# Kernel tuning notes

Measured on AMD Instinct MI355X. Metric: run time of the kernel, lower is better.

## Reference

```python
import jax, jax.numpy as jnp
import numpy as np

H = 8; D = 128; HD = D // H; T = 6; N = 512; E = 16384; FIN = 15; L = 3


def _ln(v, g, b, eps=1e-5):
    m = v.mean(-1, keepdims=True)
    var = ((v - m) ** 2).mean(-1, keepdims=True)
    return (v - m) / jnp.sqrt(var + eps) * g + b


def _gat(xn, src, dst, W, a_src, a_dst, b):
    # PyG GATConv, concat=False: lin (no bias) -> per-edge LeakyReLU scores ->
    # segment softmax over incoming edges -> scatter-sum -> head mean -> bias.
    h = (xn @ W).reshape(N, H, D)  # [N, H, D]
    e = jax.nn.leaky_relu((h * a_src).sum(-1)[src] + (h * a_dst).sum(-1)[dst], 0.2)  # [E+N, H]
    m = jax.ops.segment_max(e, dst, num_segments=N)
    ex = jnp.exp(e - m[dst])
    s = jax.ops.segment_sum(ex, dst, num_segments=N)
    a = ex / s[dst]
    out = jax.ops.segment_sum(a[..., None] * h[src], dst, num_segments=N)  # [N, H, D]
    return out.mean(1) + b


def _forward(x, edge_index, gat_W, gat_asrc, gat_adst, gat_b, ln_g, ln_b,
             enc_Wqkv, enc_bqkv, enc_Wo, enc_bo, enc_ln1g, enc_ln1b,
             enc_W1, enc_b1, enc_W2, enc_b2, enc_ln2g, enc_ln2b,
             risk_W1, risk_b1, risk_W2, risk_b2,
             mode_W1, mode_b1, mode_W2, mode_b2,
             unc_W1, unc_b1, unc_W2, unc_b2):
    B = x.shape[0]  # 1
    ar = jnp.arange(N)
    src = jnp.concatenate([edge_index[0], ar])  # PyG add_self_loops=True
    dst = jnp.concatenate([edge_index[1], ar])
    gat_t = jax.vmap(lambda xt: _gat(xt, src, dst, gat_W, gat_asrc, gat_adst, gat_b))(x[0])  # [T,N,D]
    sp = _ln(gat_t, ln_g, ln_b)
    h = sp.reshape(B, T * N, D)
    S = T * N
    for l in range(L):  # nn.TransformerEncoder, post-norm, ReLU FFN, eval mode
        qkv = h @ enc_Wqkv[l] + enc_bqkv[l]
        q, k, v = jnp.split(qkv, 3, axis=-1)
        q = q.reshape(B, S, H, HD); k = k.reshape(B, S, H, HD); v = v.reshape(B, S, H, HD)
        att = jax.nn.softmax(jnp.einsum('bqhd,bkhd->bhqk', q, k) / np.sqrt(HD).astype(np.float32), axis=-1)
        o = jnp.einsum('bhqk,bkhd->bqhd', att, v).reshape(B, S, D) @ enc_Wo[l] + enc_bo[l]
        h = _ln(h + o, enc_ln1g[l], enc_ln1b[l])
        f = jax.nn.relu(h @ enc_W1[l] + enc_b1[l]) @ enc_W2[l] + enc_b2[l]
        h = _ln(h + f, enc_ln2g[l], enc_ln2b[l])
    g = h.mean(1)  # [B, D]
    risk = jax.nn.sigmoid(jax.nn.relu(g @ risk_W1 + risk_b1) @ risk_W2 + risk_b2).squeeze()
    mode = jax.nn.relu(g @ mode_W1 + mode_b1) @ mode_W2 + mode_b2
    unc = jax.nn.softplus(jax.nn.relu(g @ unc_W1 + unc_b1) @ unc_W2 + unc_b2)
    return risk, mode, unc


def setup_inputs() -> dict:
    key = jax.random.key(0)
    ks = jax.random.split(key, 20)
    def w(i, shape, s=0.05):
        return (s * jax.random.normal(ks[i], shape)).astype(jnp.float32)
    return dict(
        x=jax.random.normal(ks[0], (1, T, N, FIN), jnp.float32),
        edge_index=jax.random.randint(ks[1], (2, E), 0, N, dtype=jnp.int32),
        gat_W=w(2, (FIN, H * D)),
        gat_asrc=w(3, (H, D)), gat_adst=w(4, (H, D)), gat_b=jnp.zeros((D,), jnp.float32),
        ln_g=jnp.ones((D,), jnp.float32), ln_b=jnp.zeros((D,), jnp.float32),
        enc_Wqkv=w(5, (L, D, 3 * D)), enc_bqkv=jnp.zeros((L, 3 * D), jnp.float32),
        enc_Wo=w(6, (L, D, D)), enc_bo=jnp.zeros((L, D), jnp.float32),
        enc_ln1g=jnp.ones((L, D), jnp.float32), enc_ln1b=jnp.zeros((L, D), jnp.float32),
        enc_W1=w(7, (L, D, 2048)), enc_b1=jnp.zeros((L, 2048), jnp.float32),
        enc_W2=w(8, (L, 2048, D)), enc_b2=jnp.zeros((L, D), jnp.float32),
        enc_ln2g=jnp.ones((L, D), jnp.float32), enc_ln2b=jnp.zeros((L, D), jnp.float32),
        risk_W1=w(9, (D, 64)), risk_b1=jnp.zeros((64,), jnp.float32),
        risk_W2=w(10, (64, 1)), risk_b2=jnp.zeros((1,), jnp.float32),
        mode_W1=w(11, (D, 32)), mode_b1=jnp.zeros((32,), jnp.float32),
        mode_W2=w(12, (32, 8)), mode_b2=jnp.zeros((8,), jnp.float32),
        unc_W1=w(13, (D, 32)), unc_b1=jnp.zeros((32,), jnp.float32),
        unc_W2=w(14, (32, 2)), unc_b2=jnp.zeros((2,), jnp.float32),
    )


def reference(x, edge_index, gat_W, gat_asrc, gat_adst, gat_b, ln_g, ln_b,
              enc_Wqkv, enc_bqkv, enc_Wo, enc_bo, enc_ln1g, enc_ln1b,
              enc_W1, enc_b1, enc_W2, enc_b2, enc_ln2g, enc_ln2b,
              risk_W1, risk_b1, risk_W2, risk_b2,
              mode_W1, mode_b1, mode_W2, mode_b2,
              unc_W1, unc_b1, unc_W2, unc_b2):
    return _forward(x, edge_index, gat_W, gat_asrc, gat_adst, gat_b, ln_g, ln_b,
                    enc_Wqkv, enc_bqkv, enc_Wo, enc_bo, enc_ln1g, enc_ln1b,
                    enc_W1, enc_b1, enc_W2, enc_b2, enc_ln2g, enc_ln2b,
                    risk_W1, risk_b1, risk_W2, risk_b2,
                    mode_W1, mode_b1, mode_W2, mode_b2,
                    unc_W1, unc_b1, unc_W2, unc_b2)
```

## Files before the change

kernel.cpp:

```cpp
#include <hip/hip_runtime.h>
#include <hip/hip_bf16.h>
#include <math.h>

#define T 6
#define N 512
#define E 16384
#define EN (E + N)
#define H 8
#define D 128
#define HD 16
#define S (T * N)
#define FIN 15
#define FF 2048
#define KS 4
#define FCH 8
#define GCH 64
#define SM_SHIFT2 2.88539008f
#define QSCALE 0.36067376f
#define VPAD2 136

typedef _Float16 half_t;
typedef _Float16 half8 __attribute__((ext_vector_type(8)));
typedef _Float16 half4 __attribute__((ext_vector_type(4)));
typedef float f32x4 __attribute__((ext_vector_type(4)));

#define MFMA16(a, b, c) __builtin_amdgcn_mfma_f32_16x16x32_f16(a, b, c, 0, 0, 0)
#define MFMA16K16(a, b, c) __builtin_amdgcn_mfma_f32_16x16x16f16(a, b, c, 0, 0, 0)

#define O_A      0
#define O_EBUF   (T*N*H*D)
#define O_C      (O_EBUF + T*EN*H)
#define O_HSEQ   (O_C + T*N*H*D)
#define O_OBUF   (O_HSEQ + S*D)
#define O_SSRC   (O_OBUF + S*D)
#define O_SDST   (O_SSRC + T*N*H)
#define O_SEGM   (O_SDST + T*N*H)
#define O_SEGS   (O_SEGM + T*N*H)
#define O_INT    (O_SEGS + T*N*H)
#define O_G      (O_INT + 20000)

#define I_DEG    0
#define I_START  512
#define I_CURS   1025
#define I_CSRE   1537

#define WB_OFF   (3*H*S*HD)
#define WB_QKV   0
#define WB_WO    147456
#define WB_W1    196608
#define WB_W2    983040

__device__ __forceinline__ float bsum(float v, float* lds, int nw) {
    #pragma unroll
    for (int off = 32; off > 0; off >>= 1) v += __shfl_down(v, off, 64);
    int w = threadIdx.x >> 6;
    if ((threadIdx.x & 63) == 0) lds[w] = v;
    __syncthreads();
    float r = 0.f;
    for (int i = 0; i < nw; ++i) r += lds[i];
    __syncthreads();
    return r;
}

__device__ __forceinline__ half_t* swz_ptr(half_t* base, int token, int col) {
    int byte = token * 256 + col * 2;
    byte ^= (token & 7) << 4;
    return (half_t*)((char*)base + byte);
}
__device__ __forceinline__ half_t* swz_ptr256(half_t* base, int token, int col) {
    int byte = token * 512 + col * 2;
    byte ^= (token & 7) << 4;
    return (half_t*)((char*)base + byte);
}

__global__ void init_kernel(float* g, int* ia) {
    int i = blockIdx.x * blockDim.x + threadIdx.x;
    if (i < D) g[i] = 0.f;
    if (i < N) ia[I_DEG + i] = 0;
}

__global__ __launch_bounds__(256) void gat_lin_kernel(
        const float* __restrict__ x, const float* __restrict__ W,
        const float* __restrict__ asrc, const float* __restrict__ adst,
        half_t* __restrict__ hbuf16, float* __restrict__ ssrc, float* __restrict__ sdst) {
    int r = blockIdx.x;
    int tid = threadIdx.x;
    __shared__ float xr[FIN];
    __shared__ float hl[H*D];
    if (tid < FIN) xr[tid] = x[r * FIN + tid];
    __syncthreads();
    #pragma unroll
    for (int kk = 0; kk < 4; ++kk) {
        int col = tid + kk * 256;
        float acc = 0.f;
        #pragma unroll
        for (int f = 0; f < FIN; ++f) acc += xr[f] * W[f * (H*D) + col];
        hbuf16[(size_t)r * (H*D) + col] = (half_t)acc;
        hl[col] = acc;
    }
    __syncthreads();
    int w = tid >> 6, lane = tid & 63;
    #pragma unroll
    for (int i = 0; i < 4; ++i) {
        int p = w*4 + i;
        int head = p >> 1;
        const float* av = ((p & 1) ? adst : asrc) + head * D;
        float v = hl[head*D + lane] * av[lane] + hl[head*D + 64 + lane] * av[64 + lane];
        #pragma unroll
        for (int off = 32; off > 0; off >>= 1) v += __shfl_down(v, off, 64);
        if (lane == 0) {
            if (p & 1) sdst[r*H + head] = v;
            else       ssrc[r*H + head] = v;
        }
    }
}

__global__ void csr_count_kernel(const int* __restrict__ ei, int* ia) {
    int j = blockIdx.x * blockDim.x + threadIdx.x;
    if (j >= EN) return;
    int dn = (j < E) ? ei[E + j] : (j - E);
    atomicAdd(&ia[I_DEG + dn], 1);
}

__global__ void csr_scan_kernel(int* ia) {
    __shared__ int buf[N];
    int tid = threadIdx.x;
    int v = ia[I_DEG + tid];
    buf[tid] = v;
    __syncthreads();
    for (int off = 1; off < N; off <<= 1) {
        int t = (tid >= off) ? buf[tid - off] : 0;
        __syncthreads();
        buf[tid] += t;
        __syncthreads();
    }
    ia[I_START + tid + 1] = buf[tid];
    if (tid == 0) ia[I_START] = 0;
    ia[I_CURS + tid] = buf[tid] - v;
}

__global__ void csr_fill_kernel(const int* __restrict__ ei, int* ia) {
    int j = blockIdx.x * blockDim.x + threadIdx.x;
    if (j >= EN) return;
    int dn = (j < E) ? ei[E + j] : (j - E);
    int slot = atomicAdd(&ia[I_CURS + dn], 1);
    ia[I_CSRE + slot] = j;
}

__global__ __launch_bounds__(128) void gat_fused_kernel(
        const int* __restrict__ ei, const int* __restrict__ ia,
        const float* __restrict__ ssrc, const float* __restrict__ sdst,
        const half_t* __restrict__ hbuf16, const float* __restrict__ gb,
        const float* __restrict__ lng, const float* __restrict__ lnb,
        float* __restrict__ hseq) {
    int bid = blockIdx.x;
    int wg = (bid & 7) * (T*N/8) + (bid >> 3);
    int t = wg / N, n = wg % N;
    int tid = threadIdx.x;
    int myh = tid & 7;

    __shared__ int snarr[GCH];
    __shared__ float earr[GCH][H];
    __shared__ float red[128];
    __shared__ float sdl[H], mS[H], sS[H], scl[H];
    __shared__ float lnred[2];

    if (tid < H) {
        sdl[tid] = sdst[(t*N + n)*H + tid];
        mS[tid] = -3.0e38f;
        sS[tid] = 0.f;
    }
    float acc[H];
    #pragma unroll
    for (int h = 0; h < H; ++h) acc[h] = 0.f;
    int e0 = ia[I_START + n], e1 = ia[I_START + n + 1];
    __syncthreads();

    for (int c0 = e0; c0 < e1; c0 += GCH) {
        int cn = min(GCH, e1 - c0);
        if (tid < cn) {
            int j = ia[I_CSRE + c0 + tid];
            snarr[tid] = (j < E) ? ei[j] : (j - E);
        }
        __syncthreads();
        float lm = -3.0e38f;
        for (int w = tid; w < cn*H; w += 128) {
            int ce = w >> 3;
            float e = ssrc[(t*N + snarr[ce])*H + myh] + sdl[myh];
            e = (e > 0.f) ? e : 0.2f * e;
            earr[ce][myh] = e;
            lm = fmaxf(lm, e);
        }
        red[tid] = lm;
        __syncthreads();
        if (tid < H) {
            float cm = red[tid];
            #pragma unroll
            for (int k = 1; k < 16; ++k) cm = fmaxf(cm, red[tid + 8*k]);
            float mn = fmaxf(mS[tid], cm);
            scl[tid] = __expf(mS[tid] - mn);
            mS[tid] = mn;
        }
        __syncthreads();
        float ls = 0.f;
        float mh = mS[myh];
        for (int w = tid; w < cn*H; w += 128) {
            int ce = w >> 3;
            float p = __expf(earr[ce][myh] - mh);
            earr[ce][myh] = p;
            ls += p;
        }
        red[tid] = ls;
        __syncthreads();
        if (tid < H) {
            float cs = red[tid];
            #pragma unroll
            for (int k = 1; k < 16; ++k) cs += red[tid + 8*k];
            sS[tid] = sS[tid] * scl[tid] + cs;
        }
        #pragma unroll
        for (int h = 0; h < H; ++h) acc[h] *= scl[h];
        for (int ce = 0; ce < cn; ++ce) {
            const half_t* hp = hbuf16 + ((size_t)(t*N + snarr[ce]) * H) * D + tid;
            #pragma unroll
            for (int h = 0; h < H; ++h)
                acc[h] += earr[ce][h] * (float)hp[(size_t)h * D];
        }
        __syncthreads();
    }

    float v = 0.f;
    #pragma unroll
    for (int h = 0; h < H; ++h) v += acc[h] / sS[h];
    v = v * (1.f / H) + gb[tid];
    float mean = bsum(v, lnred, 2) * (1.f / D);
    float diff = v - mean;
    float var = bsum(diff * diff, lnred, 2) * (1.f / D);
    hseq[(size_t)(t*N + n) * D + tid] = diff * rsqrtf(var + 1e-5f) * lng[tid] + lnb[tid];
}

__global__ __launch_bounds__(256) void wconv_kernel(
        const float* __restrict__ Wqkv, const float* __restrict__ Wo,
        const float* __restrict__ W1, const float* __restrict__ W2,
        half_t* __restrict__ WqkvT, half_t* __restrict__ WoT,
        half_t* __restrict__ W1T, half_t* __restrict__ W2T) {
    int b = blockIdx.x;
    int l = b / 576, r = b % 576;
    const float* src; half_t* dst; int Rr, Cc, tr, tc;
    if (r < 48)       { src = Wqkv + (size_t)l*128*384;  dst = WqkvT + (size_t)l*384*128;  Rr=128;  Cc=384;  tc = r % 12;        tr = r / 12; }
    else if (r < 64)  { int rr=r-48;  src = Wo + (size_t)l*128*128;  dst = WoT + (size_t)l*128*128;  Rr=128;  Cc=128;  tc = rr % 4;  tr = rr / 4; }
    else if (r < 320) { int rr=r-64;  src = W1 + (size_t)l*128*2048; dst = W1T + (size_t)l*2048*128; Rr=128;  Cc=2048; tc = rr % 64; tr = rr / 64; }
    else              { int rr=r-320; src = W2 + (size_t)l*2048*128; dst = W2T + (size_t)l*128*2048; Rr=2048; Cc=128;  tc = rr % 4;  tr = rr / 4; }
    __shared__ float t[32][33];
    int tx = threadIdx.x & 31, ty = threadIdx.x >> 5;
    #pragma unroll
    for (int i = 0; i < 4; ++i) {
        int row = tr*32 + ty + i*8, col = tc*32 + tx;
        t[ty + i*8][tx] = src[(size_t)row * Cc + col];
    }
    __syncthreads();
    #pragma unroll
    for (int i = 0; i < 4; ++i) {
        int orow = tc*32 + ty + i*8, ocol = tr*32 + tx;
        dst[(size_t)orow * Rr + ocol] = (half_t)t[tx][ty + i*8];
    }
}

__global__ __launch_bounds__(256) void qkv_mfma_kernel(
        const float* __restrict__ hseq, const half_t* __restrict__ WqkvT,
        const float* __restrict__ bqkv,
        half_t* __restrict__ Qh, half_t* __restrict__ Kh, half_t* __restrict__ Vt) {
    __shared__ half_t xt[32*128];
    int tid = threadIdx.x;
    int s0 = blockIdx.x * 32;
    for (int c = tid; c < 512; c += 256) {
        int token = c >> 4, col8 = (c & 15) * 8;
        const float* src = hseq + (size_t)(s0 + token) * 128 + col8;
        float4 a = *(const float4*)src;
        float4 b = *(const float4*)(src + 4);
        half8 v;
        v[0]=(half_t)a.x; v[1]=(half_t)a.y; v[2]=(half_t)a.z; v[3]=(half_t)a.w;
        v[4]=(half_t)b.x; v[5]=(half_t)b.y; v[6]=(half_t)b.z; v[7]=(half_t)b.w;
        *(half8*)swz_ptr(xt, token, col8) = v;
    }
    __syncthreads();
    int lane = tid & 63, w = tid >> 6;
    int lr = lane & 15, lg = lane >> 4;
    f32x4 acc[6][2];
    #pragma unroll
    for (int m = 0; m < 6; ++m)
        #pragma unroll
        for (int n = 0; n < 2; ++n) acc[m][n] = (f32x4){0.f, 0.f, 0.f, 0.f};
    #pragma unroll
    for (int ks = 0; ks < 4; ++ks) {
        half8 bf[2];
        #pragma unroll
        for (int n = 0; n < 2; ++n)
            bf[n] = *(half8*)swz_ptr(xt, n*16 + lr, ks*32 + lg*8);
        #pragma unroll
        for (int m = 0; m < 6; ++m) {
            int row = w*96 + m*16 + lr;
            half8 af = *(const half8*)(WqkvT + (size_t)row*128 + ks*32 + lg*8);
            #pragma unroll
            for (int n = 0; n < 2; ++n) acc[m][n] = MFMA16(af, bf[n], acc[m][n]);
        }
    }
    #pragma unroll
    for (int m = 0; m < 6; ++m) {
        int qd = w*96 + m*16 + lg*4;
        float4 bb = *(const float4*)(bqkv + qd);
        int part = qd >> 7, c = qd & 127, head = c >> 4, dd = c & 15;
        #pragma unroll
        for (int n = 0; n < 2; ++n) {
            int token = n*16 + lr;
            float v0 = acc[m][n][0] + bb.x, v1 = acc[m][n][1] + bb.y;
            float v2 = acc[m][n][2] + bb.z, v3 = acc[m][n][3] + bb.w;
            if (part == 0) {
                half4 hv = { (half_t)(v0*QSCALE), (half_t)(v1*QSCALE),
                             (half_t)(v2*QSCALE), (half_t)(v3*QSCALE) };
                *(half4*)(Qh + ((size_t)head*S + s0 + token)*HD + dd) = hv;
            } else if (part == 1) {
                half4 hv = { (half_t)v0, (half_t)v1, (half_t)v2, (half_t)v3 };
                *(half4*)(Kh + ((size_t)head*S + s0 + token)*HD + dd) = hv;
            } else {
                Vt[((size_t)head*HD + dd + 0)*S + s0 + token] = (half_t)v0;
                Vt[((size_t)head*HD + dd + 1)*S + s0 + token] = (half_t)v1;
                Vt[((size_t)head*HD + dd + 2)*S + s0 + token] = (half_t)v2;
                Vt[((size_t)head*HD + dd + 3)*S + s0 + token] = (half_t)v3;
            }
        }
    }
}

__global__ __launch_bounds__(256) void attn7_kernel(
        const half_t* __restrict__ Qh, const half_t* __restrict__ Kh,
        const half_t* __restrict__ Vt, float* __restrict__ pacc,
        float* __restrict__ pl) {
    int qb = blockIdx.x, h = blockIdx.y, ks = blockIdx.z;
    int tid = threadIdx.x;
    int lane = tid & 63;
    int w = tid >> 6;
    int lr = lane & 15, lg = lane >> 4;
    int qg0 = qb*128 + w*32 + lr;
    int qg1 = qg0 + 16;
    const f32x4 zf = {0.f, 0.f, 0.f, 0.f};

    __shared__ half_t kbuf[2][128*16];
    __shared__ half_t vbuf[2][16*VPAD2];

    half4 qf0 = *(const half4*)(Qh + ((size_t)h*S + qg0)*HD + lg*4);
    half4 qf1 = *(const half4*)(Qh + ((size_t)h*S + qg1)*HD + lg*4);

    int krow = tid >> 1, kch = tid & 1;
    int vdim = tid >> 4, vch = tid & 15;
    const half_t* Kbase = Kh + (size_t)h*S*HD;
    const half_t* Vbase = Vt + (size_t)h*HD*S;
    int kb0 = ks*(S/KS);

    *(half8*)&kbuf[0][krow*16 + kch*8] = *(const half8*)(Kbase + (size_t)(kb0+krow)*HD + kch*8);
    *(half8*)&vbuf[0][vdim*VPAD2 + vch*8] = *(const half8*)(Vbase + (size_t)vdim*S + kb0 + vch*8);
    __syncthreads();

    float l0 = 0.f, l1 = 0.f;
    f32x4 oa0 = zf, oa1 = zf, ob0 = zf, ob1 = zf;
    int cur = 0;
    const int NT = (S/KS)/128;
    for (int t = 0; t < NT; ++t) {
        int tn = (t+1 < NT) ? (t+1) : t;
        int kbn = kb0 + tn*128;
        half8 knext = *(const half8*)(Kbase + (size_t)(kbn+krow)*HD + kch*8);
        half8 vnext = *(const half8*)(Vbase + (size_t)vdim*S + kbn + vch*8);

        f32x4 sc0[8], sc1[8];
        #pragma unroll
        for (int ct = 0; ct < 8; ++ct) {
            half4 kf = *(half4*)&kbuf[cur][(ct*16+lr)*16 + lg*4];
            sc0[ct] = MFMA16K16(kf, qf0, zf);
            sc1[ct] = MFMA16K16(kf, qf1, zf);
        }
        half4 pf0[8], pf1[8];
        #pragma unroll
        for (int ct = 0; ct < 8; ++ct)
            #pragma unroll
            for (int r = 0; r < 4; ++r) {
                float pv0 = exp2f(sc0[ct][r] - SM_SHIFT2);
                float pv1 = exp2f(sc1[ct][r] - SM_SHIFT2);
                l0 += pv0; l1 += pv1;
                pf0[ct][r] = (half_t)pv0;
                pf1[ct][r] = (half_t)pv1;
            }
        #pragma unroll
        for (int ct = 0; ct < 8; ++ct) {
            half4 vf = *(half4*)&vbuf[cur][lr*VPAD2 + ct*16 + lg*4];
            if (ct & 1) { oa1 = MFMA16K16(vf, pf0[ct], oa1); ob1 = MFMA16K16(vf, pf1[ct], ob1); }
            else        { oa0 = MFMA16K16(vf, pf0[ct], oa0); ob0 = MFMA16K16(vf, pf1[ct], ob0); }
        }
        *(half8*)&kbuf[cur^1][krow*16 + kch*8] = knext;
        *(half8*)&vbuf[cur^1][vdim*VPAD2 + vch*8] = vnext;
        __syncthreads();
        cur ^= 1;
    }
    oa0[0]+=oa1[0]; oa0[1]+=oa1[1]; oa0[2]+=oa1[2]; oa0[3]+=oa1[3];
    ob0[0]+=ob1[0]; ob0[1]+=ob1[1]; ob0[2]+=ob1[2]; ob0[3]+=ob1[3];

    l0 += __shfl_xor(l0, 16, 64); l0 += __shfl_xor(l0, 32, 64);
    l1 += __shfl_xor(l1, 16, 64); l1 += __shfl_xor(l1, 32, 64);

    size_t oi0 = ((size_t)(ks*H + h) * S + qg0);
    size_t oi1 = ((size_t)(ks*H + h) * S + qg1);
    if (lg == 0) { pl[oi0] = l0; pl[oi1] = l1; }
    #pragma unroll
    for (int r = 0; r < 4; ++r) {
        pacc[oi0 * HD + lg*4 + r] = oa0[r];
        pacc[oi1 * HD + lg*4 + r] = ob0[r];
    }
}

__global__ __launch_bounds__(256) void oproj_mfma_ln_kernel(
        const float* __restrict__ pacc, const float* __restrict__ pl,
        const half_t* __restrict__ WoT,
        const float* __restrict__ bo, const float* __restrict__ lng,
        const float* __restrict__ lnb, float* __restrict__ hseq) {
    __shared__ half_t xt[32*128];
    __shared__ float yt[32*132];
    int tid = threadIdx.x;
    int s0 = blockIdx.x * 32;
    for (int c = tid; c < 512; c += 256) {
        int token = c >> 4, col8 = (c & 15) * 8;
        int s = s0 + token;
        int h = col8 >> 4, dd0 = col8 & 15;
        float L = 0.f;
        float a[8] = {0,0,0,0,0,0,0,0};
        #pragma unroll
        for (int k = 0; k < KS; ++k) {
            size_t oi = ((size_t)(k*H + h) * S + s);
            L += pl[oi];
            const float* pp = pacc + oi * HD + dd0;
            float4 p0 = *(const float4*)pp;
            float4 p1 = *(const float4*)(pp + 4);
            a[0]+=p0.x; a[1]+=p0.y; a[2]+=p0.z; a[3]+=p0.w;
            a[4]+=p1.x; a[5]+=p1.y; a[6]+=p1.z; a[7]+=p1.w;
        }
        float inv = 1.f / L;
        half8 v;
        #pragma unroll
        for (int i = 0; i < 8; ++i) v[i] = (half_t)(a[i] * inv);
        *(half8*)swz_ptr(xt, token, col8) = v;
    }
    __syncthreads();
    int lane = tid & 63, w = tid >> 6;
    int lr = lane & 15, lg = lane >> 4;
    f32x4 acc[2][2];
    #pragma unroll
    for (int m = 0; m < 2; ++m)
        #pragma unroll
        for (int n = 0; n < 2; ++n) acc[m][n] = (f32x4){0.f, 0.f, 0.f, 0.f};
    #pragma unroll
    for (int kk = 0; kk < 4; ++kk) {
        half8 bf[2];
        #pragma unroll
        for (int n = 0; n < 2; ++n)
            bf[n] = *(half8*)swz_ptr(xt, n*16 + lr, kk*32 + lg*8);
        #pragma unroll
        for (int m = 0; m < 2; ++m) {
            int row = w*32 + m*16 + lr;
            half8 af = *(const half8*)(WoT + (size_t)row*128 + kk*32 + lg*8);
            #pragma unroll
            for (int n = 0; n < 2; ++n) acc[m][n] = MFMA16(af, bf[n], acc[m][n]);
        }
    }
    #pragma unroll
    for (int m = 0; m < 2; ++m)
        #pragma unroll
        for (int n = 0; n < 2; ++n) {
            int token = n*16 + lr;
            int od = w*32 + m*16 + lg*4;
            *(f32x4*)&yt[token*132 + od] = acc[m][n];
        }
    __syncthreads();
    {
        int token = tid >> 3, part = tid & 7;
        const float* hres = hseq + (size_t)(s0 + token) * 128;
        float v[16];
        float sum = 0.f;
        #pragma unroll
        for (int i = 0; i < 16; ++i) {
            int dim = part*16 + i;
            v[i] = yt[token*132 + dim] + bo[dim] + hres[dim];
            sum += v[i];
        }
        sum += __shfl_xor(sum, 1, 64); sum += __shfl_xor(sum, 2, 64); sum += __shfl_xor(sum, 4, 64);
        float mean = sum * (1.f/128.f);
        float vs = 0.f;
        #pragma unroll
        for (int i = 0; i < 16; ++i) { float dq = v[i] - mean; vs += dq*dq; }
        vs += __shfl_xor(vs, 1, 64); vs += __shfl_xor(vs, 2, 64); vs += __shfl_xor(vs, 4, 64);
        float inv = rsqrtf(vs * (1.f/128.f) + 1e-5f);
        #pragma unroll
        for (int i = 0; i < 16; ++i) {
            int dim = part*16 + i;
            hseq[(size_t)(s0+token)*128 + dim] = (v[i]-mean)*inv*lng[dim] + lnb[dim];
        }
    }
}

__global__ __launch_bounds__(256) void ffn_mfma2_kernel(
        const half_t* __restrict__ W1T, const half_t* __restrict__ W2T,
        const float* __restrict__ b1, const float* __restrict__ hseq,
        float* __restrict__ ypart) {
    __shared__ half_t xt[32*128];
    __shared__ half_t h1[32*256];
    int tid = threadIdx.x;
    int s0 = blockIdx.x * 32;
    int fc = blockIdx.y;
    int fbase = fc * 256;
    for (int c = tid; c < 512; c += 256) {
        int token = c >> 4, col8 = (c & 15) * 8;
        const float* src = hseq + (size_t)(s0 + token) * 128 + col8;
        float4 a = *(const float4*)src;
        float4 b = *(const float4*)(src + 4);
        half8 v;
        v[0]=(half_t)a.x; v[1]=(half_t)a.y; v[2]=(half_t)a.z; v[3]=(half_t)a.w;
        v[4]=(half_t)b.x; v[5]=(half_t)b.y; v[6]=(half_t)b.z; v[7]=(half_t)b.w;
        *(half8*)swz_ptr(xt, token, col8) = v;
    }
    __syncthreads();
    int lane = tid & 63, mw = tid >> 6;
    int lr = lane & 15, lg = lane >> 4;

    f32x4 hacc[4][2];
    #pragma unroll
    for (int m = 0; m < 4; ++m)
        #pragma unroll
        for (int n = 0; n < 2; ++n) hacc[m][n] = (f32x4){0.f, 0.f, 0.f, 0.f};
    #pragma unroll
    for (int ksx = 0; ksx < 4; ++ksx) {
        half8 bf[2];
        #pragma unroll
        for (int n = 0; n < 2; ++n)
            bf[n] = *(half8*)swz_ptr(xt, n*16 + lr, ksx*32 + lg*8);
        #pragma unroll
        for (int m = 0; m < 4; ++m) {
            int row = fbase + mw*64 + m*16 + lr;
            half8 af = *(const half8*)(W1T + (size_t)row*128 + ksx*32 + lg*8);
            #pragma unroll
            for (int n = 0; n < 2; ++n) hacc[m][n] = MFMA16(af, bf[n], hacc[m][n]);
        }
    }
    #pragma unroll
    for (int m = 0; m < 4; ++m) {
        int frow = mw*64 + m*16 + lg*4;
        float4 bb = *(const float4*)(b1 + fbase + frow);
        #pragma unroll
        for (int n = 0; n < 2; ++n) {
            int token = n*16 + lr;
            half4 hv;
            hv[0] = (half_t)fmaxf(hacc[m][n][0] + bb.x, 0.f);
            hv[1] = (half_t)fmaxf(hacc[m][n][1] + bb.y, 0.f);
            hv[2] = (half_t)fmaxf(hacc[m][n][2] + bb.z, 0.f);
            hv[3] = (half_t)fmaxf(hacc[m][n][3] + bb.w, 0.f);
            *(half4*)swz_ptr256(h1, token, frow) = hv;
        }
    }
    __syncthreads();

    f32x4 yacc[2][2];
    #pragma unroll
    for (int m = 0; m < 2; ++m)
        #pragma unroll
        for (int n = 0; n < 2; ++n) yacc[m][n] = (f32x4){0.f, 0.f, 0.f, 0.f};
    #pragma unroll
    for (int ksx = 0; ksx < 8; ++ksx) {
        half8 bf[2];
        #pragma unroll
        for (int n = 0; n < 2; ++n)
            bf[n] = *(half8*)swz_ptr256(h1, n*16 + lr, ksx*32 + lg*8);
        #pragma unroll
        for (int m = 0; m < 2; ++m) {
            int row = mw*32 + m*16 + lr;
            half8 af = *(const half8*)(W2T + (size_t)row*2048 + fbase + ksx*32 + lg*8);
            #pragma unroll
            for (int n = 0; n < 2; ++n) yacc[m][n] = MFMA16(af, bf[n], yacc[m][n]);
        }
    }
    #pragma unroll
    for (int m = 0; m < 2; ++m)
        #pragma unroll
        for (int n = 0; n < 2; ++n) {
            int token = n*16 + lr;
            int od = mw*32 + m*16 + lg*4;
            *(f32x4*)&ypart[((size_t)fc*S + s0 + token)*128 + od] = yacc[m][n];
        }
}

__global__ __launch_bounds__(256) void ffn_reduce_ln_kernel(
        const float* __restrict__ ypart, const float* __restrict__ b2,
        const float* __restrict__ lng, const float* __restrict__ lnb,
        float* __restrict__ hseq) {
    int tid = threadIdx.x;
    int token = blockIdx.x * 64 + (tid >> 2);
    int part = tid & 3;
    const float* hres = hseq + (size_t)token * 128;
    float v[32];
    #pragma unroll
    for (int i = 0; i < 32; ++i) {
        int dim = part*32 + i;
        v[i] = b2[dim] + hres[dim];
    }
    #pragma unroll
    for (int fcc = 0; fcc < FCH; ++fcc) {
        const float* yp = ypart + ((size_t)fcc*S + token)*128 + part*32;
        #pragma unroll
        for (int i = 0; i < 32; ++i) v[i] += yp[i];
    }
    float sum = 0.f;
    #pragma unroll
    for (int i = 0; i < 32; ++i) sum += v[i];
    sum += __shfl_xor(sum, 1, 64); sum += __shfl_xor(sum, 2, 64);
    float mean = sum * (1.f/128.f);
    float vs = 0.f;
    #pragma unroll
    for (int i = 0; i < 32; ++i) { float dq = v[i] - mean; vs += dq*dq; }
    vs += __shfl_xor(vs, 1, 64); vs += __shfl_xor(vs, 2, 64);
    float inv = rsqrtf(vs * (1.f/128.f) + 1e-5f);
    #pragma unroll
    for (int i = 0; i < 32; ++i) {
        int dim = part*32 + i;
        hseq[(size_t)token*128 + dim] = (v[i]-mean)*inv*lng[dim] + lnb[dim];
    }
}

__global__ void pool_kernel(const float* __restrict__ hseq, float* __restrict__ g) {
    int d = threadIdx.x;
    int b = blockIdx.x;
    float acc = 0.f;
    for (int s = b * 128; s < (b + 1) * 128; ++s) acc += hseq[s * D + d];
    atomicAdd(&g[d], acc * (1.f / S));
}

__global__ void heads_kernel(const float* __restrict__ g,
                             const float* __restrict__ rW1, const float* __restrict__ rb1,
                             const float* __restrict__ rW2, const float* __restrict__ rb2,
                             const float* __restrict__ mW1, const float* __restrict__ mb1,
                             const float* __restrict__ mW2, const float* __restrict__ mb2,
                             const float* __restrict__ uW1, const float* __restrict__ ub1,
                             const float* __restrict__ uW2, const float* __restrict__ ub2,
                             float* __restrict__ out) {
    int tid = threadIdx.x;
    __shared__ float gl[D];
    __shared__ float r1[64];
    __shared__ float mh[32];
    __shared__ float uh[32];
    gl[tid] = g[tid];
    gl[tid + 64] = g[tid + 64];
    __syncthreads();
    {
        float acc = rb1[tid];
        for (int k = 0; k < D; ++k) acc += gl[k] * rW1[k * 64 + tid];
        r1[tid] = fmaxf(acc, 0.f);
    }
    if (tid < 32) {
        float am = mb1[tid], au = ub1[tid];
        for (int k = 0; k < D; ++k) {
            am += gl[k] * mW1[k * 32 + tid];
            au += gl[k] * uW1[k * 32 + tid];
        }
        mh[tid] = fmaxf(am, 0.f);
        uh[tid] = fmaxf(au, 0.f);
    }
    __syncthreads();
    if (tid == 0) {
        float acc = rb2[0];
        for (int k = 0; k < 64; ++k) acc += r1[k] * rW2[k];
        out[0] = 1.f / (1.f + __expf(-acc));
    }
    if (tid < 8) {
        float acc = mb2[tid];
        for (int k = 0; k < 32; ++k) acc += mh[k] * mW2[k * 8 + tid];
        out[1 + tid] = acc;
    }
    if (tid < 2) {
        float acc = ub2[tid];
        for (int k = 0; k < 32; ++k) acc += uh[k] * uW2[k * 2 + tid];
        out[9 + tid] = (acc > 20.f) ? acc : log1pf(__expf(acc));
    }
}

extern "C" void kernel_launch(void* const* d_in, const int* in_sizes, int n_in,
                              void* d_out, int out_size, void* d_ws, size_t ws_size,
                              hipStream_t stream) {
    const float* x       = (const float*)d_in[0];
    const int*   ei      = (const int*)  d_in[1];
    const float* gat_W   = (const float*)d_in[2];
    const float* gat_asrc= (const float*)d_in[3];
    const float* gat_adst= (const float*)d_in[4];
    const float* gat_b   = (const float*)d_in[5];
    const float* ln_g    = (const float*)d_in[6];
    const float* ln_b    = (const float*)d_in[7];
    const float* Wqkv    = (const float*)d_in[8];
    const float* bqkv    = (const float*)d_in[9];
    const float* Wo      = (const float*)d_in[10];
    const float* bo      = (const float*)d_in[11];
    const float* ln1g    = (const float*)d_in[12];
    const float* ln1b    = (const float*)d_in[13];
    const float* W1      = (const float*)d_in[14];
    const float* b1      = (const float*)d_in[15];
    const float* W2      = (const float*)d_in[16];
    const float* b2      = (const float*)d_in[17];
    const float* ln2g    = (const float*)d_in[18];
    const float* ln2b    = (const float*)d_in[19];
    const float* rW1     = (const float*)d_in[20];
    const float* rb1     = (const float*)d_in[21];
    const float* rW2     = (const float*)d_in[22];
    const float* rb2     = (const float*)d_in[23];
    const float* mW1     = (const float*)d_in[24];
    const float* mb1     = (const float*)d_in[25];
    const float* mW2     = (const float*)d_in[26];
    const float* mb2     = (const float*)d_in[27];
    const float* uW1     = (const float*)d_in[28];
    const float* ub1     = (const float*)d_in[29];
    const float* uW2     = (const float*)d_in[30];
    const float* ub2     = (const float*)d_in[31];

    float* ws = (float*)d_ws;
    half_t*       hbuf16 = (half_t*)(ws + O_A);
    half_t*       Qh   = (half_t*)(ws + O_A);
    half_t*       Kh   = Qh + (size_t)H*S*HD;
    half_t*       Vt   = Kh + (size_t)H*S*HD;
    half_t*       wb   = (half_t*)(ws + O_A + WB_OFF);
    half_t*       WqkvT= wb + WB_QKV;
    half_t*       WoT  = wb + WB_WO;
    half_t*       W1T  = wb + WB_W1;
    half_t*       W2T  = wb + WB_W2;
    float*        pacc = ws + O_C;
    float*        ypart= ws + O_C;
    float*        pl   = ws + O_C + (size_t)KS*H*S*HD;
    float*        hseq = ws + O_HSEQ;
    float*        ssrc = ws + O_SSRC;
    float*        sdst = ws + O_SDST;
    int*          ia   = (int*)(ws + O_INT);
    float*        gvec = ws + O_G;
    float* out = (float*)d_out;

    init_kernel<<<dim3(2), dim3(256), 0, stream>>>(gvec, ia);

    gat_lin_kernel<<<dim3(T*N), dim3(256), 0, stream>>>(x, gat_W, gat_asrc, gat_adst,
                                                        hbuf16, ssrc, sdst);
    csr_count_kernel<<<dim3((EN + 255) / 256), dim3(256), 0, stream>>>(ei, ia);
    csr_scan_kernel<<<dim3(1), dim3(N), 0, stream>>>(ia);
    csr_fill_kernel<<<dim3((EN + 255) / 256), dim3(256), 0, stream>>>(ei, ia);
    gat_fused_kernel<<<dim3(T*N), dim3(128), 0, stream>>>(
        ei, ia, ssrc, sdst, hbuf16, gat_b, ln_g, ln_b, hseq);

    wconv_kernel<<<dim3(3*576), dim3(256), 0, stream>>>(Wqkv, Wo, W1, W2, WqkvT, WoT, W1T, W2T);

    for (int l = 0; l < 3; ++l) {
        qkv_mfma_kernel<<<dim3(S/32), dim3(256), 0, stream>>>(
            hseq, WqkvT + (size_t)l*384*128, bqkv + l*3*D, Qh, Kh, Vt);
        attn7_kernel<<<dim3(S/128, H, KS), dim3(256), 0, stream>>>(Qh, Kh, Vt, pacc, pl);
        oproj_mfma_ln_kernel<<<dim3(S/32), dim3(256), 0, stream>>>(
            pacc, pl, WoT + (size_t)l*128*128, bo + l*D, ln1g + l*D, ln1b + l*D, hseq);
        ffn_mfma2_kernel<<<dim3(S/32, FCH), dim3(256), 0, stream>>>(
            W1T + (size_t)l*2048*128, W2T + (size_t)l*128*2048,
            b1 + l*FF, hseq, ypart);
        ffn_reduce_ln_kernel<<<dim3(S/64), dim3(256), 0, stream>>>(
            ypart, b2 + l*D, ln2g + l*D, ln2b + l*D, hseq);
    }

    pool_kernel<<<dim3(S / 128), dim3(128), 0, stream>>>(hseq, gvec);
    heads_kernel<<<dim3(1), dim3(64), 0, stream>>>(gvec, rW1, rb1, rW2, rb2,
                                                   mW1, mb1, mW2, mb2,
                                                   uW1, ub1, uW2, ub2, out);
}
```

Measured before the change: 332.8 us.

## Fuse FFN reduce+LayerNorm into next QKV kernel and CSR count into GAT linear

Measured after the change: 303.2 us. 1.1x faster.

```diff
diff --git a/kernel.cpp b/kernel.cpp
--- a/kernel.cpp
+++ b/kernel.cpp
@@ -82,9 +82,15 @@
 __global__ __launch_bounds__(256) void gat_lin_kernel(
         const float* __restrict__ x, const float* __restrict__ W,
         const float* __restrict__ asrc, const float* __restrict__ adst,
+        const int* __restrict__ ei, int* __restrict__ ia,
         half_t* __restrict__ hbuf16, float* __restrict__ ssrc, float* __restrict__ sdst) {
     int r = blockIdx.x;
     int tid = threadIdx.x;
+    int j = r * 256 + tid;
+    if (r < (EN + 255) / 256 && j < EN) {
+        int dn = (j < E) ? ei[E + j] : (j - E);
+        atomicAdd(&ia[I_DEG + dn], 1);
+    }
     __shared__ float xr[FIN];
     __shared__ float hl[H*D];
     if (tid < FIN) xr[tid] = x[r * FIN + tid];
@@ -113,13 +119,6 @@
             else       ssrc[r*H + head] = v;
         }
     }
-}
-
-__global__ void csr_count_kernel(const int* __restrict__ ei, int* ia) {
-    int j = blockIdx.x * blockDim.x + threadIdx.x;
-    if (j >= EN) return;
-    int dn = (j < E) ? ei[E + j] : (j - E);
-    atomicAdd(&ia[I_DEG + dn], 1);
 }
 
 __global__ void csr_scan_kernel(int* ia) {
@@ -267,21 +266,58 @@
 }
 
 __global__ __launch_bounds__(256) void qkv_mfma_kernel(
-        const float* __restrict__ hseq, const half_t* __restrict__ WqkvT,
-        const float* __restrict__ bqkv,
+        float* __restrict__ hseq, const float* __restrict__ ypart,
+        const float* __restrict__ b2, const float* __restrict__ lng2,
+        const float* __restrict__ lnb2, int doRed,
+        const half_t* __restrict__ WqkvT, const float* __restrict__ bqkv,
         half_t* __restrict__ Qh, half_t* __restrict__ Kh, half_t* __restrict__ Vt) {
     __shared__ half_t xt[32*128];
     int tid = threadIdx.x;
     int s0 = blockIdx.x * 32;
-    for (int c = tid; c < 512; c += 256) {
-        int token = c >> 4, col8 = (c & 15) * 8;
-        const float* src = hseq + (size_t)(s0 + token) * 128 + col8;
-        float4 a = *(const float4*)src;
-        float4 b = *(const float4*)(src + 4);
-        half8 v;
-        v[0]=(half_t)a.x; v[1]=(half_t)a.y; v[2]=(half_t)a.z; v[3]=(half_t)a.w;
-        v[4]=(half_t)b.x; v[5]=(half_t)b.y; v[6]=(half_t)b.z; v[7]=(half_t)b.w;
-        *(half8*)swz_ptr(xt, token, col8) = v;
+    if (doRed) {
+        int token = tid >> 3, part = tid & 7;
+        int s = s0 + token;
+        const float* hres = hseq + (size_t)s * 128;
+        float v[16];
+        #pragma unroll
+        for (int i = 0; i < 16; ++i) v[i] = b2[part*16 + i] + hres[part*16 + i];
+        #pragma unroll
+        for (int fcc = 0; fcc < FCH; ++fcc) {
+            const float* yp = ypart + ((size_t)fcc*S + s)*128 + part*16;
+            #pragma unroll
+            for (int i = 0; i < 16; ++i) v[i] += yp[i];
+        }
+        float sum = 0.f;
+        #pragma unroll
+        for (int i = 0; i < 16; ++i) sum += v[i];
+        sum += __shfl_xor(sum, 1, 64); sum += __shfl_xor(sum, 2, 64); sum += __shfl_xor(sum, 4, 64);
+        float mean = sum * (1.f/128.f);
+        float vs = 0.f;
+        #pragma unroll
+        for (int i = 0; i < 16; ++i) { float dq = v[i] - mean; vs += dq*dq; }
+        vs += __shfl_xor(vs, 1, 64); vs += __shfl_xor(vs, 2, 64); vs += __shfl_xor(vs, 4, 64);
+        float inv = rsqrtf(vs * (1.f/128.f) + 1e-5f);
+        half8 o0, o1;
+        #pragma unroll
+        for (int i = 0; i < 16; ++i) {
+            int dim = part*16 + i;
+            float ov = (v[i]-mean)*inv*lng2[dim] + lnb2[dim];
+            hseq[(size_t)s*128 + dim] = ov;
+            if (i < 8) o0[i] = (half_t)ov; else o1[i-8] = (half_t)ov;
+        }
+        *(half8*)swz_ptr(xt, token, part*16) = o0;
+        *(half8*)swz_ptr(xt, token, part*16 + 8) = o1;
+    } else {
+        for (int c = tid; c < 512; c += 256) {
+            int token = c >> 4, col8 = (c & 15) * 8;
+            const float* src = hseq + (size_t)(s0 + token) * 128 + col8;
+            float4 a = *(const float4*)src;
+            float4 b = *(const float4*)(src + 4);
+            half8 v;
+            v[0]=(half_t)a.x; v[1]=(half_t)a.y; v[2]=(half_t)a.z; v[3]=(half_t)a.w;
+            v[4]=(half_t)b.x; v[5]=(half_t)b.y; v[6]=(half_t)b.z; v[7]=(half_t)b.w;
+            *(half8*)swz_ptr(xt, token, col8) = v;
+        }
     }
     __syncthreads();
     int lane = tid & 63, w = tid >> 6;
@@ -366,10 +402,12 @@
     int cur = 0;
     const int NT = (S/KS)/128;
     for (int t = 0; t < NT; ++t) {
-        int tn = (t+1 < NT) ? (t+1) : t;
-        int kbn = kb0 + tn*128;
-        half8 knext = *(const half8*)(Kbase + (size_t)(kbn+krow)*HD + kch*8);
-        half8 vnext = *(const half8*)(Vbase + (size_t)vdim*S + kbn + vch*8);
+        half8 knext, vnext;
+        if (t+1 < NT) {
+            int kbn = kb0 + (t+1)*128;
+            knext = *(const half8*)(Kbase + (size_t)(kbn+krow)*HD + kch*8);
+            vnext = *(const half8*)(Vbase + (size_t)vdim*S + kbn + vch*8);
+        }
 
         f32x4 sc0[8], sc1[8];
         #pragma unroll
@@ -395,10 +433,12 @@
             if (ct & 1) { oa1 = MFMA16K16(vf, pf0[ct], oa1); ob1 = MFMA16K16(vf, pf1[ct], ob1); }
             else        { oa0 = MFMA16K16(vf, pf0[ct], oa0); ob0 = MFMA16K16(vf, pf1[ct], ob0); }
         }
-        *(half8*)&kbuf[cur^1][krow*16 + kch*8] = knext;
-        *(half8*)&vbuf[cur^1][vdim*VPAD2 + vch*8] = vnext;
-        __syncthreads();
-        cur ^= 1;
+        if (t+1 < NT) {
+            *(half8*)&kbuf[cur^1][krow*16 + kch*8] = knext;
+            *(half8*)&vbuf[cur^1][vdim*VPAD2 + vch*8] = vnext;
+            __syncthreads();
+            cur ^= 1;
+        }
     }
     oa0[0]+=oa1[0]; oa0[1]+=oa1[1]; oa0[2]+=oa1[2]; oa0[3]+=oa1[3];
     ob0[0]+=ob1[0]; ob0[1]+=ob1[1]; ob0[2]+=ob1[2]; ob0[3]+=ob1[3];
@@ -745,8 +785,7 @@
     init_kernel<<<dim3(2), dim3(256), 0, stream>>>(gvec, ia);
 
     gat_lin_kernel<<<dim3(T*N), dim3(256), 0, stream>>>(x, gat_W, gat_asrc, gat_adst,
-                                                        hbuf16, ssrc, sdst);
-    csr_count_kernel<<<dim3((EN + 255) / 256), dim3(256), 0, stream>>>(ei, ia);
+                                                        ei, ia, hbuf16, ssrc, sdst);
     csr_scan_kernel<<<dim3(1), dim3(N), 0, stream>>>(ia);
     csr_fill_kernel<<<dim3((EN + 255) / 256), dim3(256), 0, stream>>>(ei, ia);
     gat_fused_kernel<<<dim3(T*N), dim3(128), 0, stream>>>(
@@ -756,16 +795,17 @@
 
     for (int l = 0; l < 3; ++l) {
         qkv_mfma_kernel<<<dim3(S/32), dim3(256), 0, stream>>>(
-            hseq, WqkvT + (size_t)l*384*128, bqkv + l*3*D, Qh, Kh, Vt);
+            hseq, ypart, b2 + (l-1)*D, ln2g + (l-1)*D, ln2b + (l-1)*D, (l > 0) ? 1 : 0,
+            WqkvT + (size_t)l*384*128, bqkv + l*3*D, Qh, Kh, Vt);
         attn7_kernel<<<dim3(S/128, H, KS), dim3(256), 0, stream>>>(Qh, Kh, Vt, pacc, pl);
         oproj_mfma_ln_kernel<<<dim3(S/32), dim3(256), 0, stream>>>(
             pacc, pl, WoT + (size_t)l*128*128, bo + l*D, ln1g + l*D, ln1b + l*D, hseq);
         ffn_mfma2_kernel<<<dim3(S/32, FCH), dim3(256), 0, stream>>>(
             W1T + (size_t)l*2048*128, W2T + (size_t)l*128*2048,
             b1 + l*FF, hseq, ypart);
-        ffn_reduce_ln_kernel<<<dim3(S/64), dim3(256), 0, stream>>>(
-            ypart, b2 + l*D, ln2g + l*D, ln2b + l*D, hseq);
-    }
+    }
+    ffn_reduce_ln_kernel<<<dim3(S/64), dim3(256), 0, stream>>>(
+        ypart, b2 + 2*D, ln2g + 2*D, ln2b + 2*D, hseq);
 
     pool_kernel<<<dim3(S / 128), dim3(128), 0, stream>>>(hseq, gvec);
     heads_kernel<<<dim3(1), dim3(64), 0, stream>>>(gvec, rW1, rb1, rW2, rb2,
```
